# Performance work log

Hardware: AMD Instinct MI355X
Metric: run time of the kernel (lower is better)

## Reference

```python
import jax, jax.numpy as jnp
import numpy as np

N, D, R, NB, E = 50000, 128, 16, 10, 1600000
DECAY_RATE = 0.1
LN_EPS = 1e-5

def setup_inputs() -> dict:
    key = jax.random.key(0)
    ks = jax.random.split(key, 12)
    x = jax.random.normal(ks[0], (N, D), dtype=jnp.float32)
    edge_index = jax.random.randint(ks[1], (2, E), 0, N, dtype=jnp.int64)
    edge_type = jax.random.randint(ks[2], (E,), 0, R, dtype=jnp.int64)
    edge_time = jax.random.uniform(ks[3], (E,), dtype=jnp.float32)
    s = 1.0 / np.sqrt(D)
    basis = jax.random.normal(ks[4], (NB, D, D), dtype=jnp.float32) * s   # RGCN basis matrices
    comp = jax.random.normal(ks[5], (R, NB), dtype=jnp.float32) * (1.0 / np.sqrt(NB))
    root = jax.random.normal(ks[6], (D, D), dtype=jnp.float32) * s        # RGCN self-loop weight
    bias = jnp.zeros((D,), dtype=jnp.float32)
    tp_w = jax.random.normal(ks[7], (D, D), dtype=jnp.float32) * s        # time_proj
    tp_b = jnp.zeros((D,), dtype=jnp.float32)
    gamma = jnp.ones((D,), dtype=jnp.float32)
    beta = jnp.zeros((D,), dtype=jnp.float32)
    return {"x": x, "edge_index": edge_index, "edge_type": edge_type, "edge_time": edge_time,
            "basis": basis, "comp": comp, "root": root, "bias": bias,
            "tp_w": tp_w, "tp_b": tp_b, "gamma": gamma, "beta": beta}

def reference(x, edge_index, edge_type, edge_time, basis, comp, root, bias, tp_w, tp_b, gamma, beta):
    n, d = x.shape
    r = comp.shape[0]
    src, dst = edge_index[0], edge_index[1]
    # ---- RGCNConv (basis decomposition, per-relation mean aggregation) ----
    W = jnp.einsum('rb,bio->rio', comp, basis)                 # [R, D, D]
    msg = x[src]                                               # [E, D] gather
    seg = dst * r + edge_type                                  # combined (node, relation) segment id
    agg = jax.ops.segment_sum(msg, seg, num_segments=n * r)    # [N*R, D]
    cnt = jax.ops.segment_sum(jnp.ones_like(seg, dtype=x.dtype), seg, num_segments=n * r)
    agg = (agg / jnp.maximum(cnt, 1.0)[:, None]).reshape(n, r, d)  # per-relation mean
    x_rgcn = jnp.einsum('nrd,rdo->no', agg, W) + x @ root + bias
    # ---- exponential time decay weights, normalized to sum 1 ----
    td = edge_time.max() - edge_time
    td = td / (td.max() + 1e-8)
    w = jnp.exp(-DECAY_RATE * td)
    w = w / (w.sum() + 1e-8)
    # ---- time-decay aggregation (sum over relations == single scatter-add) ----
    agg_t = jax.ops.segment_sum(msg * w[:, None], dst, num_segments=n)
    deg = jax.ops.segment_sum(jnp.ones_like(dst, dtype=x.dtype), dst, num_segments=n)
    x_time = agg_t / jnp.clip(deg, 1.0)[:, None]
    # ---- combine, relu, (dropout=identity in eval), layernorm ----
    xc = x_rgcn + x_time @ tp_w + tp_b
    h = jax.nn.relu(xc)
    mu = h.mean(-1, keepdims=True)
    var = ((h - mu) ** 2).mean(-1, keepdims=True)
    return (h - mu) * jax.lax.rsqrt(var + LN_EPS) * gamma + beta
```

## Files before the change

kernel.cpp:

```cpp
#include <hip/hip_runtime.h>
#include <hip/hip_bf16.h>
#include <math.h>

#define NN 50000
#define DD 128
#define RR 16
#define NBASIS 10
#define NE 1600000
#define NSEG (NN * RR)
#define NSLICE 12
#define KTOT (NSLICE * DD)
#define DECAY 0.1f

#define NB_COARSE 782
#define NBLK_S 1024
#define EPB 1563
#define NHC (NB_COARSE * NBLK_S)
#define NPART2 (NHC / 1024)
#define FINE 1024
#define CAP 2560

typedef short bf16x8 __attribute__((ext_vector_type(8)));
typedef float f32x4 __attribute__((ext_vector_type(4)));
typedef float f32x2 __attribute__((ext_vector_type(2)));

__device__ __forceinline__ ushort f2b(float f) {
    unsigned u = __float_as_uint(f);
    unsigned r = (u + 0x7FFFu + ((u >> 16) & 1u)) >> 16;
    return (ushort)r;
}
__device__ __forceinline__ unsigned cvt_pk_bf16(float lo, float hi) {
    unsigned r;
    asm("v_cvt_pk_bf16_f32 %0, %1, %2" : "=v"(r) : "v"(lo), "v"(hi));
    return r;
}


#define XB_ITEMS (NN * (DD / 4))
#define PREP_ITEMS (XB_ITEMS + DD * KTOT)
__global__ __launch_bounds__(256) void k_s1(
    const int* __restrict__ edst, const float* __restrict__ t,
    const float* __restrict__ x, const float* __restrict__ basis,
    const float* __restrict__ root, const float* __restrict__ tp_w,
    unsigned* __restrict__ red, unsigned* __restrict__ Hc,
    ushort* __restrict__ xb, ushort* __restrict__ Bt3)
{
    const int bid = blockIdx.x;
    const int tid = threadIdx.x;
    if (bid < NBLK_S) {
        __shared__ unsigned h[NB_COARSE];
        for (int i = tid; i < NB_COARSE; i += 256) h[i] = 0u;
        __syncthreads();
        const int e0 = bid * EPB;
        const int e1 = (e0 + EPB < NE) ? e0 + EPB : NE;
        for (int e = e0 + tid; e < e1; e += 256) {
            int d = __builtin_nontemporal_load(edst + e);
            atomicAdd(&h[d >> 6], 1u);
        }
        __syncthreads();
        for (int i = tid; i < NB_COARSE; i += 256)
            Hc[i * NBLK_S + bid] = h[i];
        return;
    }
    if (bid < NBLK_S + 256) {
        __shared__ float smx[4], smn[4];
        float mx = 0.0f, mn = 1e30f;
        const int stride = 256 * 256;
        for (int i = (bid - NBLK_S) * 256 + tid; i < NE / 4; i += stride) {
            f32x4 v = __builtin_nontemporal_load(((const f32x4*)t) + i);
            mx = fmaxf(mx, fmaxf(fmaxf(v.x, v.y), fmaxf(v.z, v.w)));
            mn = fminf(mn, fminf(fminf(v.x, v.y), fminf(v.z, v.w)));
        }
        for (int o = 32; o >= 1; o >>= 1) {
            mx = fmaxf(mx, __shfl_down(mx, o, 64));
            mn = fminf(mn, __shfl_down(mn, o, 64));
        }
        if ((tid & 63) == 0) { smx[tid >> 6] = mx; smn[tid >> 6] = mn; }
        __syncthreads();
        if (tid == 0) {
            mx = fmaxf(fmaxf(smx[0], smx[1]), fmaxf(smx[2], smx[3]));
            mn = fminf(fminf(smn[0], smn[1]), fminf(smn[2], smn[3]));
            atomicMax(&red[0], __float_as_uint(mx));
            atomicMax(&red[1], ~__float_as_uint(mn));
        }
        return;
    }
    int idx = (bid - NBLK_S - 256) * 256 + tid;
    if (idx < XB_ITEMS) {
        f32x4 v = ((const f32x4*)x)[idx];
        uint2 o;
        o.x = cvt_pk_bf16(v.x, v.y);
        o.y = cvt_pk_bf16(v.z, v.w);
        ((uint2*)xb)[idx] = o;
        return;
    }
    int bidx = idx - XB_ITEMS;
    if (bidx >= DD * KTOT) return;
    int j = bidx / KTOT, k = bidx - j * KTOT;
    int s = k >> 7, d = k & 127;
    float v;
    if (s < NBASIS) {
        v = basis[(s * DD + d) * DD + j];
    } else if (s == NBASIS) {
        v = tp_w[d * DD + j];
    } else {
        v = root[d * DD + j];
    }
    Bt3[bidx] = f2b(v);
}

__global__ __launch_bounds__(1024) void k_scan1(unsigned* __restrict__ Hc,
                                                unsigned* __restrict__ part) {
    __shared__ unsigned sh[1024];
    int tid = threadIdx.x;
    int i = blockIdx.x * 1024 + tid;
    unsigned v = Hc[i];
    sh[tid] = v;
    __syncthreads();
    for (int off = 1; off < 1024; off <<= 1) {
        unsigned t = (tid >= off) ? sh[tid - off] : 0u;
        __syncthreads();
        sh[tid] += t;
        __syncthreads();
    }
    Hc[i] = sh[tid] - v;
    if (tid == 1023) part[blockIdx.x] = sh[1023];
}

__global__ __launch_bounds__(1024) void k_scan2(unsigned* __restrict__ part) {
    __shared__ unsigned sh[1024];
    int tid = threadIdx.x;
    unsigned v = (tid < NPART2) ? part[tid] : 0u;
    sh[tid] = v;
    __syncthreads();
    for (int off = 1; off < 1024; off <<= 1) {
        unsigned t = (tid >= off) ? sh[tid - off] : 0u;
        __syncthreads();
        sh[tid] += t;
        __syncthreads();
    }
    if (tid < NPART2) part[tid] = sh[tid] - v;
}

__global__ __launch_bounds__(1024) void k_scan3(unsigned* __restrict__ Hc,
                                                const unsigned* __restrict__ part) {
    int i = blockIdx.x * 1024 + threadIdx.x;
    Hc[i] += part[i >> 10];
}

__global__ __launch_bounds__(256) void k_s3(
    const int* __restrict__ esrc, const int* __restrict__ edst,
    const int* __restrict__ etype, const float* __restrict__ etime,
    const unsigned* __restrict__ Hc, unsigned* __restrict__ red,
    unsigned long long* __restrict__ tmp)
{
    __shared__ unsigned cur[NB_COARSE];
    __shared__ float ssum[4];
    const int bid = blockIdx.x;
    const int tid = threadIdx.x;
    for (int i = tid; i < NB_COARSE; i += 256)
        cur[i] = Hc[i * NBLK_S + bid];
    const float tmax = __uint_as_float(red[0]);
    const float tmin = __uint_as_float(~red[1]);
    const float rtd = -DECAY / (tmax - tmin + 1e-8f);
    __syncthreads();
    float s = 0.0f;
    const int e0 = bid * EPB;
    const int e1 = (e0 + EPB < NE) ? e0 + EPB : NE;
    for (int e = e0 + tid; e < e1; e += 256) {
        int d    = __builtin_nontemporal_load(edst + e);
        int ty   = __builtin_nontemporal_load(etype + e);
        int sv   = __builtin_nontemporal_load(esrc + e);
        float tv = __builtin_nontemporal_load(etime + e);
        float w = __expf((tmax - tv) * rtd);
        s += w;
        unsigned seg = (unsigned)(d * RR + ty);
        unsigned pos = atomicAdd(&cur[seg >> 10], 1u);
        unsigned lo = (unsigned)(sv & 0xFFFF) | ((unsigned)f2b(w) << 16);
        __builtin_nontemporal_store(
            ((unsigned long long)seg << 32) | lo, tmp + pos);
    }
    for (int o = 32; o >= 1; o >>= 1) s += __shfl_down(s, o, 64);
    if ((tid & 63) == 0) ssum[tid >> 6] = s;
    __syncthreads();
    if (tid == 0)
        atomicAdd(((float*)red) + 2, ssum[0] + ssum[1] + ssum[2] + ssum[3]);
}

__global__ __launch_bounds__(512) void k_s4(
    const unsigned long long* __restrict__ tmp, const unsigned* __restrict__ Hc,
    unsigned* __restrict__ srcw, unsigned* __restrict__ segptr)
{
    __shared__ unsigned long long recs[CAP];
    __shared__ unsigned hist[FINE];
    __shared__ unsigned excl[FINE];
    __shared__ unsigned curf[FINE];
    __shared__ unsigned sh[512];
    const int b = blockIdx.x;
    const int tid = threadIdx.x;
    const unsigned start = Hc[b * NBLK_S];
    const unsigned end   = (b + 1 < NB_COARSE) ? Hc[(b + 1) * NBLK_S] : (unsigned)NE;
    int n = (int)(end - start);
    if (n > CAP) n = CAP;
    for (int i = tid; i < FINE; i += 512) hist[i] = 0u;
    for (int i = tid; i < n; i += 512) recs[i] = tmp[start + i];
    __syncthreads();
    const unsigned base = (unsigned)b << 10;
    for (int i = tid; i < n; i += 512)
        atomicAdd(&hist[(unsigned)(recs[i] >> 32) - base], 1u);
    __syncthreads();
    unsigned a0 = hist[2 * tid], a1 = hist[2 * tid + 1];
    sh[tid] = a0 + a1;
    __syncthreads();
    for (int off = 1; off < 512; off <<= 1) {
        unsigned t = (tid >= off) ? sh[tid - off] : 0u;
        __syncthreads();
        sh[tid] += t;
        __syncthreads();
    }
    unsigned pe = sh[tid] - (a0 + a1);
    excl[2 * tid] = pe;          curf[2 * tid] = pe;
    excl[2 * tid + 1] = pe + a0; curf[2 * tid + 1] = pe + a0;
    __syncthreads();
    for (int i = tid; i < n; i += 512) {
        unsigned long long r = recs[i];
        unsigned p = atomicAdd(&curf[(unsigned)(r >> 32) - base], 1u);
        srcw[start + p] = (unsigned)r;
    }
    for (int i = tid; i < FINE; i += 512)
        segptr[(size_t)b * FINE + i] = start + excl[i];
}

__global__ __launch_bounds__(256) void k_gather(
    const ushort* __restrict__ xb, const unsigned* __restrict__ srcw,
    const unsigned* __restrict__ segptr, const unsigned* __restrict__ red,
    const float* __restrict__ comp,
    ushort* __restrict__ A2)
{
    const int wave = threadIdx.x >> 6, lane = threadIdx.x & 63;
    int dst0 = blockIdx.x * 4 + wave;
    if (dst0 >= NN) return;
    const int dst = __builtin_amdgcn_readfirstlane(dst0);
    const float sumw = ((const float*)red)[2];
    const unsigned s0 = (unsigned)dst * RR;
    const unsigned start = segptr[s0];
    const unsigned endAll = segptr[s0 + RR];
    const unsigned deg = endAll - start;
    unsigned* arow = (unsigned*)(A2 + (size_t)dst * KTOT);
    const unsigned* xbu = (const unsigned*)xb;

    f32x2 cb[NBASIS];
#pragma unroll
    for (int b = 0; b < NBASIS; ++b) cb[b] = (f32x2){0.f, 0.f};
    f32x2 acc = {0.f, 0.f}, xt = {0.f, 0.f};

    int r = 0;
    unsigned scur = start;
    unsigned endr = segptr[s0 + 1];
    unsigned e = start;

#define FLUSH_REL {                                                          \
        float scl = (endr > scur) ? (1.0f / (float)(endr - scur)) : 0.0f;    \
        f32x2 t = acc * scl;                                                 \
        _Pragma("unroll")                                                    \
        for (int b = 0; b < NBASIS; ++b)                                     \
            cb[b] += t * comp[r * NBASIS + b];                               \
        acc = (f32x2){0.f, 0.f}; scur = endr; ++r;                           \
        endr = (r < RR) ? segptr[s0 + r + 1] : 0xFFFFFFFFu; }

#define ACCUM(recq, pvq) {                                                   \
        float wgt = __uint_as_float((recq) & 0xFFFF0000u);                   \
        f32x2 v;                                                             \
        v.x = __uint_as_float((pvq) << 16);                                  \
        v.y = __uint_as_float((pvq) & 0xFFFF0000u);                          \
        acc += v;                                                            \
        xt += v * wgt; }

    while (e < endAll) {
        unsigned idx = e + (unsigned)lane;
        unsigned recv = srcw[(idx < endAll) ? idx : (endAll - 1u)];
        unsigned chunk = endAll - e;
        if (chunk > 64u) chunk = 64u;
        unsigned j = 0;
        for (; j + 8u <= chunk; j += 8u) {
            unsigned rec0 = (unsigned)__builtin_amdgcn_readlane((int)recv, (int)(j + 0));
            unsigned rec1 = (unsigned)__builtin_amdgcn_readlane((int)recv, (int)(j + 1));
            unsigned rec2 = (unsigned)__builtin_amdgcn_readlane((int)recv, (int)(j + 2));
            unsigned rec3 = (unsigned)__builtin_amdgcn_readlane((int)recv, (int)(j + 3));
            unsigned rec4 = (unsigned)__builtin_amdgcn_readlane((int)recv, (int)(j + 4));
            unsigned rec5 = (unsigned)__builtin_amdgcn_readlane((int)recv, (int)(j + 5));
            unsigned rec6 = (unsigned)__builtin_amdgcn_readlane((int)recv, (int)(j + 6));
            unsigned rec7 = (unsigned)__builtin_amdgcn_readlane((int)recv, (int)(j + 7));
            unsigned pv0 = xbu[((rec0 & 0xFFFFu) << 6) + lane];
            unsigned pv1 = xbu[((rec1 & 0xFFFFu) << 6) + lane];
            unsigned pv2 = xbu[((rec2 & 0xFFFFu) << 6) + lane];
            unsigned pv3 = xbu[((rec3 & 0xFFFFu) << 6) + lane];
            unsigned pv4 = xbu[((rec4 & 0xFFFFu) << 6) + lane];
            unsigned pv5 = xbu[((rec5 & 0xFFFFu) << 6) + lane];
            unsigned pv6 = xbu[((rec6 & 0xFFFFu) << 6) + lane];
            unsigned pv7 = xbu[((rec7 & 0xFFFFu) << 6) + lane];
            while (e >= endr) FLUSH_REL; ACCUM(rec0, pv0); ++e;
            while (e >= endr) FLUSH_REL; ACCUM(rec1, pv1); ++e;
            while (e >= endr) FLUSH_REL; ACCUM(rec2, pv2); ++e;
            while (e >= endr) FLUSH_REL; ACCUM(rec3, pv3); ++e;
            while (e >= endr) FLUSH_REL; ACCUM(rec4, pv4); ++e;
            while (e >= endr) FLUSH_REL; ACCUM(rec5, pv5); ++e;
            while (e >= endr) FLUSH_REL; ACCUM(rec6, pv6); ++e;
            while (e >= endr) FLUSH_REL; ACCUM(rec7, pv7); ++e;
        }
        for (; j < chunk; ++j) {
            unsigned rc = (unsigned)__builtin_amdgcn_readlane((int)recv, (int)j);
            unsigned pv = xbu[((rc & 0xFFFFu) << 6) + lane];
            while (e >= endr) FLUSH_REL;
            ACCUM(rc, pv);
            ++e;
        }
    }
    while (r < RR) FLUSH_REL;

#pragma unroll
    for (int b = 0; b < NBASIS; ++b)
        __builtin_nontemporal_store(cvt_pk_bf16(cb[b].x, cb[b].y),
                                    arow + b * 64 + lane);

    float s2 = 1.0f / ((sumw + 1e-8f) * fmaxf((float)deg, 1.0f));
    __builtin_nontemporal_store(cvt_pk_bf16(xt.x * s2, xt.y * s2),
                                arow + NBASIS * 64 + lane);
    __builtin_nontemporal_store(
        ((const unsigned*)(xb + (size_t)dst * DD))[lane],
        arow + (NBASIS + 1) * 64 + lane);
#undef FLUSH_REL
#undef ACCUM
}

__global__ __launch_bounds__(256) void k_fgemm(
    const ushort* __restrict__ A2, const ushort* __restrict__ Bt3,
    const float* __restrict__ bias, const float* __restrict__ tpb,
    const float* __restrict__ gamma, const float* __restrict__ beta,
    float* __restrict__ out)
{
    __shared__ unsigned Bs[2][4096];

    const int tid = threadIdx.x;
    const int w = tid >> 6, lane = tid & 63;
    const int quad = lane >> 4, l16 = lane & 15;
    const int n0 = blockIdx.x * 64;

    f32x4 acc[8];
#pragma unroll
    for (int ct = 0; ct < 8; ++ct) acc[ct] = (f32x4){0.f, 0.f, 0.f, 0.f};

    const ushort* arow = A2 + (size_t)(n0 + w * 16 + l16) * KTOT + quad * 8;
    const int srow = lane >> 3;
    const int sc   = lane & 7;

#define STAGE(buf, itv) {                                                    \
        const int k0_ = (itv) * 64;                                          \
        _Pragma("unroll")                                                    \
        for (int i_ = 0; i_ < 4; ++i_) {                                     \
            const int cid_ = i_ * 4 + w;                                     \
            const int row_ = cid_ * 8 + srow;                                \
            const int ck_  = sc ^ (row_ & 7);                                \
            const ushort* gb_ = Bt3 + (size_t)row_ * KTOT + k0_ + ck_ * 8;   \
            __builtin_amdgcn_global_load_lds(                                \
                (const __attribute__((address_space(1))) unsigned*)gb_,      \
                (__attribute__((address_space(3))) unsigned*)&Bs[buf][cid_ * 256], \
                16, 0, 0);                                                   \
        } }

    STAGE(0, 0);
    bf16x8 afp0 = *(const bf16x8*)(arow);
    bf16x8 afp1 = *(const bf16x8*)(arow + 32);
    __syncthreads();

    const int NIT = KTOT / 64;
    for (int it = 0; it < NIT; ++it) {
        if (it + 1 < NIT) STAGE((it + 1) & 1, it + 1);
        bf16x8 af0 = afp0, af1 = afp1;
        if (it + 1 < NIT) {
            afp0 = *(const bf16x8*)(arow + (it + 1) * 64);
            afp1 = *(const bf16x8*)(arow + (it + 1) * 64 + 32);
        }
        const unsigned* Bp = &Bs[it & 1][0];
#pragma unroll
        for (int ct = 0; ct < 8; ++ct) {
            const int rB = ct * 16 + l16;
            bf16x8 b0 = *(const bf16x8*)&Bp[rB * 32 + ((quad ^ (rB & 7)) << 2)];
            bf16x8 b1 = *(const bf16x8*)&Bp[rB * 32 + (((4 + quad) ^ (rB & 7)) << 2)];
            acc[ct] = __builtin_amdgcn_mfma_f32_16x16x32_bf16(af0, b0, acc[ct], 0, 0, 0);
            acc[ct] = __builtin_amdgcn_mfma_f32_16x16x32_bf16(af1, b1, acc[ct], 0, 0, 0);
        }
        __syncthreads();
    }
#undef STAGE

    float bc[8], gc[8], be[8];
#pragma unroll
    for (int ct = 0; ct < 8; ++ct) {
        int col = ct * 16 + l16;
        bc[ct] = bias[col] + tpb[col];
        gc[ct] = gamma[col];
        be[ct] = beta[col];
    }
    float s[4] = {0, 0, 0, 0}, q[4] = {0, 0, 0, 0};
#pragma unroll
    for (int ct = 0; ct < 8; ++ct)
#pragma unroll
        for (int i = 0; i < 4; ++i) {
            float v = fmaxf(acc[ct][i] + bc[ct], 0.0f);
            acc[ct][i] = v;
            s[i] += v;
            q[i] = fmaf(v, v, q[i]);
        }
#pragma unroll
    for (int off = 1; off < 16; off <<= 1)
#pragma unroll
        for (int i = 0; i < 4; ++i) {
            s[i] += __shfl_xor(s[i], off, 64);
            q[i] += __shfl_xor(q[i], off, 64);
        }
#pragma unroll
    for (int i = 0; i < 4; ++i) {
        const int row = n0 + w * 16 + quad * 4 + i;
        float mu  = s[i] * (1.0f / DD);
        float var = q[i] * (1.0f / DD) - mu * mu;
        float inv = rsqrtf(var + 1e-5f);
        if (row < NN) {
#pragma unroll
            for (int ct = 0; ct < 8; ++ct)
                __builtin_nontemporal_store(
                    (acc[ct][i] - mu) * inv * gc[ct] + be[ct],
                    out + (size_t)row * DD + ct * 16 + l16);
        }
    }
}

extern "C" void kernel_launch(void* const* d_in, const int* in_sizes, int n_in,
                              void* d_out, int out_size, void* d_ws, size_t ws_size,
                              hipStream_t stream)
{
    const float* x     = (const float*)d_in[0];
    const int*   ei    = (const int*)d_in[1];
    const int*   etype = (const int*)d_in[2];
    const float* etime = (const float*)d_in[3];
    const float* basis = (const float*)d_in[4];
    const float* comp  = (const float*)d_in[5];
    const float* root  = (const float*)d_in[6];
    const float* bias  = (const float*)d_in[7];
    const float* tp_w  = (const float*)d_in[8];
    const float* tp_b  = (const float*)d_in[9];
    const float* gamma = (const float*)d_in[10];
    const float* beta  = (const float*)d_in[11];
    float* out = (float*)d_out;

    char* ws = (char*)d_ws;
    size_t off = 0;
    auto alloc = [&](size_t bytes) -> void* {
        void* p = ws + off;
        off = (off + bytes + 255) & ~(size_t)255;
        return p;
    };
    unsigned* red    = (unsigned*)alloc(256);
    unsigned* Hc     = (unsigned*)alloc((size_t)NHC * 4);
    unsigned* part   = (unsigned*)alloc(1024 * 4);
    unsigned* srcw   = (unsigned*)alloc((size_t)NE * 4);
    unsigned long long* tmp = (unsigned long long*)alloc((size_t)NE * 8);
    unsigned* segptr = (unsigned*)alloc((size_t)(NB_COARSE * FINE) * 4);
    ushort*   xb     = (ushort*)alloc((size_t)NN * DD * 2);
    ushort*   Bt3    = (ushort*)alloc((size_t)DD * KTOT * 2);
    ushort*   A2     = (ushort*)alloc((size_t)50048 * KTOT * 2);
    (void)ws_size;

    const int* esrc = ei;
    const int* edst = ei + NE;

    (void)hipMemsetAsync(red, 0, 256, stream);

    const int prep_blocks = (PREP_ITEMS + 255) / 256;
    hipLaunchKernelGGL(k_s1, dim3(NBLK_S + 256 + prep_blocks), dim3(256), 0, stream,
                       edst, etime, x, basis, root, tp_w, red, Hc, xb, Bt3);

    hipLaunchKernelGGL(k_scan1, dim3(NPART2), dim3(1024), 0, stream, Hc, part);
    hipLaunchKernelGGL(k_scan2, dim3(1), dim3(1024), 0, stream, part);
    hipLaunchKernelGGL(k_scan3, dim3(NPART2), dim3(1024), 0, stream, Hc, part);

    hipLaunchKernelGGL(k_s3, dim3(NBLK_S), dim3(256), 0, stream,
                       esrc, edst, etype, etime, Hc, red, tmp);

    hipLaunchKernelGGL(k_s4, dim3(NB_COARSE), dim3(512), 0, stream,
                       tmp, Hc, srcw, segptr);

    hipLaunchKernelGGL(k_gather, dim3((NN + 3) / 4), dim3(256), 0, stream,
                       xb, srcw, segptr, red, comp, A2);

    hipLaunchKernelGGL(k_fgemm, dim3((50048 + 63) / 64), dim3(256), 0, stream,
                       A2, Bt3, bias, tp_b, gamma, beta, out);
}
```

Before: 344.7 us.

## Fuse gather and GEMM+LayerNorm into one kernel using LDS-staged A rows

Merges the gather kernel and the fused GEMM/LayerNorm kernel into one 1024-thread block kernel. Each block gathers 16 destination rows into padded LDS, then 16 waves split the 128 output columns and two K halves and run MFMA with B read straight from global memory. Partial sums and LayerNorm statistics are reduced through LDS. This removes the write and re-read of the large A2 intermediate, but B is no longer staged in LDS and is reloaded by every block, and occupancy may fall because of the large blocks and LDS use.

```diff
diff --git a/kernel.cpp b/kernel.cpp
--- a/kernel.cpp
+++ b/kernel.cpp
@@ -7,7 +7,6 @@
 #define RR 16
 #define NBASIS 10
 #define NE 1600000
-#define NSEG (NN * RR)
 #define NSLICE 12
 #define KTOT (NSLICE * DD)
 #define DECAY 0.1f
@@ -19,6 +18,8 @@
 #define NPART2 (NHC / 1024)
 #define FINE 1024
 #define CAP 2560
+
+#define APAD 772
 
 typedef short bf16x8 __attribute__((ext_vector_type(8)));
 typedef float f32x4 __attribute__((ext_vector_type(4)));
@@ -231,41 +232,49 @@
         segptr[(size_t)b * FINE + i] = start + excl[i];
 }
 
-__global__ __launch_bounds__(256) void k_gather(
+__global__ __launch_bounds__(1024, 4) void k_gg(
     const ushort* __restrict__ xb, const unsigned* __restrict__ srcw,
     const unsigned* __restrict__ segptr, const unsigned* __restrict__ red,
-    const float* __restrict__ comp,
-    ushort* __restrict__ A2)
+    const float* __restrict__ comp, const ushort* __restrict__ Bt3,
+    const float* __restrict__ bias, const float* __restrict__ tpb,
+    const float* __restrict__ gamma, const float* __restrict__ beta,
+    float* __restrict__ out)
 {
-    const int wave = threadIdx.x >> 6, lane = threadIdx.x & 63;
-    int dst0 = blockIdx.x * 4 + wave;
-    if (dst0 >= NN) return;
-    const int dst = __builtin_amdgcn_readfirstlane(dst0);
-    const float sumw = ((const float*)red)[2];
-    const unsigned s0 = (unsigned)dst * RR;
-    const unsigned start = segptr[s0];
-    const unsigned endAll = segptr[s0 + RR];
-    const unsigned deg = endAll - start;
-    unsigned* arow = (unsigned*)(A2 + (size_t)dst * KTOT);
-    const unsigned* xbu = (const unsigned*)xb;
-
-    f32x2 cb[NBASIS];
-#pragma unroll
-    for (int b = 0; b < NBASIS; ++b) cb[b] = (f32x2){0.f, 0.f};
-    f32x2 acc = {0.f, 0.f}, xt = {0.f, 0.f};
-
-    int r = 0;
-    unsigned scur = start;
-    unsigned endr = segptr[s0 + 1];
-    unsigned e = start;
+    __shared__ unsigned As[16 * APAD];
+    __shared__ f32x4 racc[8][64];
+    __shared__ float rs[128], rq[128];
+
+    const int tid = threadIdx.x;
+    const int w = tid >> 6, lane = tid & 63;
+    const int l16 = lane & 15, quad = lane >> 4;
+
+    {
+        const int dst = __builtin_amdgcn_readfirstlane(blockIdx.x * 16 + w);
+        const float sumw = ((const float*)red)[2];
+        const unsigned s0 = (unsigned)dst * RR;
+        const unsigned start = segptr[s0];
+        const unsigned endAll = segptr[s0 + RR];
+        const unsigned deg = endAll - start;
+        unsigned* arow = &As[w * APAD];
+        const unsigned* xbu = (const unsigned*)xb;
+
+        f32x2 cb[NBASIS];
+#pragma unroll
+        for (int b = 0; b < NBASIS; ++b) cb[b] = (f32x2){0.f, 0.f};
+        f32x2 acc2 = {0.f, 0.f}, xt = {0.f, 0.f};
+
+        int r = 0;
+        unsigned scur = start;
+        unsigned endr = segptr[s0 + 1];
+        unsigned e = start;
 
 #define FLUSH_REL {                                                          \
         float scl = (endr > scur) ? (1.0f / (float)(endr - scur)) : 0.0f;    \
-        f32x2 t = acc * scl;                                                 \
+        f32x2 t = acc2 * scl;                                                \
         _Pragma("unroll")                                                    \
         for (int b = 0; b < NBASIS; ++b)                                     \
             cb[b] += t * comp[r * NBASIS + b];                               \
-        acc = (f32x2){0.f, 0.f}; scur = endr; ++r;                           \
+        acc2 = (f32x2){0.f, 0.f}; scur = endr; ++r;                          \
         endr = (r < RR) ? segptr[s0 + r + 1] : 0xFFFFFFFFu; }
 
 #define ACCUM(recq, pvq) {                                                   \
@@ -273,145 +282,89 @@
         f32x2 v;                                                             \
         v.x = __uint_as_float((pvq) << 16);                                  \
         v.y = __uint_as_float((pvq) & 0xFFFF0000u);                          \
-        acc += v;                                                            \
+        acc2 += v;                                                           \
         xt += v * wgt; }
 
-    while (e < endAll) {
-        unsigned idx = e + (unsigned)lane;
-        unsigned recv = srcw[(idx < endAll) ? idx : (endAll - 1u)];
-        unsigned chunk = endAll - e;
-        if (chunk > 64u) chunk = 64u;
-        unsigned j = 0;
-        for (; j + 8u <= chunk; j += 8u) {
-            unsigned rec0 = (unsigned)__builtin_amdgcn_readlane((int)recv, (int)(j + 0));
-            unsigned rec1 = (unsigned)__builtin_amdgcn_readlane((int)recv, (int)(j + 1));
-            unsigned rec2 = (unsigned)__builtin_amdgcn_readlane((int)recv, (int)(j + 2));
-            unsigned rec3 = (unsigned)__builtin_amdgcn_readlane((int)recv, (int)(j + 3));
-            unsigned rec4 = (unsigned)__builtin_amdgcn_readlane((int)recv, (int)(j + 4));
-            unsigned rec5 = (unsigned)__builtin_amdgcn_readlane((int)recv, (int)(j + 5));
-            unsigned rec6 = (unsigned)__builtin_amdgcn_readlane((int)recv, (int)(j + 6));
-            unsigned rec7 = (unsigned)__builtin_amdgcn_readlane((int)recv, (int)(j + 7));
-            unsigned pv0 = xbu[((rec0 & 0xFFFFu) << 6) + lane];
-            unsigned pv1 = xbu[((rec1 & 0xFFFFu) << 6) + lane];
-            unsigned pv2 = xbu[((rec2 & 0xFFFFu) << 6) + lane];
-            unsigned pv3 = xbu[((rec3 & 0xFFFFu) << 6) + lane];
-            unsigned pv4 = xbu[((rec4 & 0xFFFFu) << 6) + lane];
-            unsigned pv5 = xbu[((rec5 & 0xFFFFu) << 6) + lane];
-            unsigned pv6 = xbu[((rec6 & 0xFFFFu) << 6) + lane];
-            unsigned pv7 = xbu[((rec7 & 0xFFFFu) << 6) + lane];
-            while (e >= endr) FLUSH_REL; ACCUM(rec0, pv0); ++e;
-            while (e >= endr) FLUSH_REL; ACCUM(rec1, pv1); ++e;
-            while (e >= endr) FLUSH_REL; ACCUM(rec2, pv2); ++e;
-            while (e >= endr) FLUSH_REL; ACCUM(rec3, pv3); ++e;
-            while (e >= endr) FLUSH_REL; ACCUM(rec4, pv4); ++e;
-            while (e >= endr) FLUSH_REL; ACCUM(rec5, pv5); ++e;
-            while (e >= endr) FLUSH_REL; ACCUM(rec6, pv6); ++e;
-            while (e >= endr) FLUSH_REL; ACCUM(rec7, pv7); ++e;
-        }
-        for (; j < chunk; ++j) {
-            unsigned rc = (unsigned)__builtin_amdgcn_readlane((int)recv, (int)j);
-            unsigned pv = xbu[((rc & 0xFFFFu) << 6) + lane];
-            while (e >= endr) FLUSH_REL;
-            ACCUM(rc, pv);
-            ++e;
-        }
-    }
-    while (r < RR) FLUSH_REL;
-
-#pragma unroll
-    for (int b = 0; b < NBASIS; ++b)
-        __builtin_nontemporal_store(cvt_pk_bf16(cb[b].x, cb[b].y),
-                                    arow + b * 64 + lane);
-
-    float s2 = 1.0f / ((sumw + 1e-8f) * fmaxf((float)deg, 1.0f));
-    __builtin_nontemporal_store(cvt_pk_bf16(xt.x * s2, xt.y * s2),
-                                arow + NBASIS * 64 + lane);
-    __builtin_nontemporal_store(
-        ((const unsigned*)(xb + (size_t)dst * DD))[lane],
-        arow + (NBASIS + 1) * 64 + lane);
+        while (e < endAll) {
+            unsigned idx = e + (unsigned)lane;
+            unsigned recv = srcw[(idx < endAll) ? idx : (endAll - 1u)];
+            unsigned chunk = endAll - e;
+            if (chunk > 64u) chunk = 64u;
+            unsigned j = 0;
+            for (; j + 8u <= chunk; j += 8u) {
+                unsigned rec0 = (unsigned)__builtin_amdgcn_readlane((int)recv, (int)(j + 0));
+                unsigned rec1 = (unsigned)__builtin_amdgcn_readlane((int)recv, (int)(j + 1));
+                unsigned rec2 = (unsigned)__builtin_amdgcn_readlane((int)recv, (int)(j + 2));
+                unsigned rec3 = (unsigned)__builtin_amdgcn_readlane((int)recv, (int)(j + 3));
+                unsigned rec4 = (unsigned)__builtin_amdgcn_readlane((int)recv, (int)(j + 4));
+                unsigned rec5 = (unsigned)__builtin_amdgcn_readlane((int)recv, (int)(j + 5));
+                unsigned rec6 = (unsigned)__builtin_amdgcn_readlane((int)recv, (int)(j + 6));
+                unsigned rec7 = (unsigned)__builtin_amdgcn_readlane((int)recv, (int)(j + 7));
+                unsigned pv0 = xbu[((rec0 & 0xFFFFu) << 6) + lane];
+                unsigned pv1 = xbu[((rec1 & 0xFFFFu) << 6) + lane];
+                unsigned pv2 = xbu[((rec2 & 0xFFFFu) << 6) + lane];
+                unsigned pv3 = xbu[((rec3 & 0xFFFFu) << 6) + lane];
+                unsigned pv4 = xbu[((rec4 & 0xFFFFu) << 6) + lane];
+                unsigned pv5 = xbu[((rec5 & 0xFFFFu) << 6) + lane];
+                unsigned pv6 = xbu[((rec6 & 0xFFFFu) << 6) + lane];
+                unsigned pv7 = xbu[((rec7 & 0xFFFFu) << 6) + lane];
+                while (e >= endr) FLUSH_REL; ACCUM(rec0, pv0); ++e;
+                while (e >= endr) FLUSH_REL; ACCUM(rec1, pv1); ++e;
+                while (e >= endr) FLUSH_REL; ACCUM(rec2, pv2); ++e;
+                while (e >= endr) FLUSH_REL; ACCUM(rec3, pv3); ++e;
+                while (e >= endr) FLUSH_REL; ACCUM(rec4, pv4); ++e;
+                while (e >= endr) FLUSH_REL; ACCUM(rec5, pv5); ++e;
+                while (e >= endr) FLUSH_REL; ACCUM(rec6, pv6); ++e;
+                while (e >= endr) FLUSH_REL; ACCUM(rec7, pv7); ++e;
+            }
+            for (; j < chunk; ++j) {
+                unsigned rc = (unsigned)__builtin_amdgcn_readlane((int)recv, (int)j);
+                unsigned pv = xbu[((rc & 0xFFFFu) << 6) + lane];
+                while (e >= endr) FLUSH_REL;
+                ACCUM(rc, pv);
+                ++e;
+            }
+        }
+        while (r < RR) FLUSH_REL;
+
+#pragma unroll
+        for (int b = 0; b < NBASIS; ++b)
+            arow[b * 64 + lane] = cvt_pk_bf16(cb[b].x, cb[b].y);
+        float s2 = 1.0f / ((sumw + 1e-8f) * fmaxf((float)deg, 1.0f));
+        arow[NBASIS * 64 + lane] = cvt_pk_bf16(xt.x * s2, xt.y * s2);
+        arow[(NBASIS + 1) * 64 + lane] =
+            ((const unsigned*)(xb + (size_t)dst * DD))[lane];
 #undef FLUSH_REL
 #undef ACCUM
-}
-
-__global__ __launch_bounds__(256) void k_fgemm(
-    const ushort* __restrict__ A2, const ushort* __restrict__ Bt3,
-    const float* __restrict__ bias, const float* __restrict__ tpb,
-    const float* __restrict__ gamma, const float* __restrict__ beta,
-    float* __restrict__ out)
-{
-    __shared__ unsigned Bs[2][4096];
-
-    const int tid = threadIdx.x;
-    const int w = tid >> 6, lane = tid & 63;
-    const int quad = lane >> 4, l16 = lane & 15;
-    const int n0 = blockIdx.x * 64;
-
-    f32x4 acc[8];
-#pragma unroll
-    for (int ct = 0; ct < 8; ++ct) acc[ct] = (f32x4){0.f, 0.f, 0.f, 0.f};
-
-    const ushort* arow = A2 + (size_t)(n0 + w * 16 + l16) * KTOT + quad * 8;
-    const int srow = lane >> 3;
-    const int sc   = lane & 7;
-
-#define STAGE(buf, itv) {                                                    \
-        const int k0_ = (itv) * 64;                                          \
-        _Pragma("unroll")                                                    \
-        for (int i_ = 0; i_ < 4; ++i_) {                                     \
-            const int cid_ = i_ * 4 + w;                                     \
-            const int row_ = cid_ * 8 + srow;                                \
-            const int ck_  = sc ^ (row_ & 7);                                \
-            const ushort* gb_ = Bt3 + (size_t)row_ * KTOT + k0_ + ck_ * 8;   \
-            __builtin_amdgcn_global_load_lds(                                \
-                (const __attribute__((address_space(1))) unsigned*)gb_,      \
-                (__attribute__((address_space(3))) unsigned*)&Bs[buf][cid_ * 256], \
-                16, 0, 0);                                                   \
-        } }
-
-    STAGE(0, 0);
-    bf16x8 afp0 = *(const bf16x8*)(arow);
-    bf16x8 afp1 = *(const bf16x8*)(arow + 32);
-    __syncthreads();
-
-    const int NIT = KTOT / 64;
-    for (int it = 0; it < NIT; ++it) {
-        if (it + 1 < NIT) STAGE((it + 1) & 1, it + 1);
-        bf16x8 af0 = afp0, af1 = afp1;
-        if (it + 1 < NIT) {
-            afp0 = *(const bf16x8*)(arow + (it + 1) * 64);
-            afp1 = *(const bf16x8*)(arow + (it + 1) * 64 + 32);
-        }
-        const unsigned* Bp = &Bs[it & 1][0];
-#pragma unroll
-        for (int ct = 0; ct < 8; ++ct) {
-            const int rB = ct * 16 + l16;
-            bf16x8 b0 = *(const bf16x8*)&Bp[rB * 32 + ((quad ^ (rB & 7)) << 2)];
-            bf16x8 b1 = *(const bf16x8*)&Bp[rB * 32 + (((4 + quad) ^ (rB & 7)) << 2)];
-            acc[ct] = __builtin_amdgcn_mfma_f32_16x16x32_bf16(af0, b0, acc[ct], 0, 0, 0);
-            acc[ct] = __builtin_amdgcn_mfma_f32_16x16x32_bf16(af1, b1, acc[ct], 0, 0, 0);
-        }
-        __syncthreads();
-    }
-#undef STAGE
-
-    float bc[8], gc[8], be[8];
-#pragma unroll
-    for (int ct = 0; ct < 8; ++ct) {
-        int col = ct * 16 + l16;
-        bc[ct] = bias[col] + tpb[col];
-        gc[ct] = gamma[col];
-        be[ct] = beta[col];
-    }
-    float s[4] = {0, 0, 0, 0}, q[4] = {0, 0, 0, 0};
-#pragma unroll
-    for (int ct = 0; ct < 8; ++ct)
-#pragma unroll
-        for (int i = 0; i < 4; ++i) {
-            float v = fmaxf(acc[ct][i] + bc[ct], 0.0f);
-            acc[ct][i] = v;
-            s[i] += v;
-            q[i] = fmaf(v, v, q[i]);
-        }
+    }
+    __syncthreads();
+
+    const int ct = w & 7, kh = w >> 3;
+    const int col = ct * 16 + l16;
+    f32x4 acc = (f32x4){0.f, 0.f, 0.f, 0.f};
+    {
+        const ushort* bcol = Bt3 + (size_t)col * KTOT + kh * 768 + quad * 8;
+        const int abase = l16 * APAD + kh * 384 + quad * 4;
+#pragma unroll
+        for (int kc = 0; kc < 24; ++kc) {
+            bf16x8 af = *(const bf16x8*)&As[abase + kc * 16];
+            bf16x8 bf = *(const bf16x8*)(bcol + kc * 32);
+            acc = __builtin_amdgcn_mfma_f32_16x16x32_bf16(af, bf, acc, 0, 0, 0);
+        }
+    }
+
+    if (w >= 8) racc[ct][lane] = acc;
+    __syncthreads();
+    if (w < 8) acc += racc[ct][lane];
+
+    float bc = bias[col] + tpb[col];
+    float gc = gamma[col], be = beta[col];
+    float s[4], q[4];
+#pragma unroll
+    for (int i = 0; i < 4; ++i) {
+        float v = fmaxf(acc[i] + bc, 0.0f);
+        acc[i] = v; s[i] = v; q[i] = v * v;
+    }
 #pragma unroll
     for (int off = 1; off < 16; off <<= 1)
 #pragma unroll
@@ -419,18 +372,27 @@
             s[i] += __shfl_xor(s[i], off, 64);
             q[i] += __shfl_xor(q[i], off, 64);
         }
-#pragma unroll
-    for (int i = 0; i < 4; ++i) {
-        const int row = n0 + w * 16 + quad * 4 + i;
-        float mu  = s[i] * (1.0f / DD);
-        float var = q[i] * (1.0f / DD) - mu * mu;
-        float inv = rsqrtf(var + 1e-5f);
-        if (row < NN) {
-#pragma unroll
-            for (int ct = 0; ct < 8; ++ct)
-                __builtin_nontemporal_store(
-                    (acc[ct][i] - mu) * inv * gc[ct] + be[ct],
-                    out + (size_t)row * DD + ct * 16 + l16);
+    if (w < 8 && l16 == 0) {
+#pragma unroll
+        for (int i = 0; i < 4; ++i) {
+            rs[ct * 16 + quad * 4 + i] = s[i];
+            rq[ct * 16 + quad * 4 + i] = q[i];
+        }
+    }
+    __syncthreads();
+    if (w < 8) {
+#pragma unroll
+        for (int i = 0; i < 4; ++i) {
+            const int rowl = quad * 4 + i;
+            float S = 0.f, Q = 0.f;
+#pragma unroll
+            for (int c = 0; c < 8; ++c) { S += rs[c * 16 + rowl]; Q += rq[c * 16 + rowl]; }
+            float mu  = S * (1.0f / DD);
+            float var = Q * (1.0f / DD) - mu * mu;
+            float inv = rsqrtf(var + 1e-5f);
+            __builtin_nontemporal_store(
+                (acc[i] - mu) * inv * gc + be,
+                out + (size_t)(blockIdx.x * 16 + rowl) * DD + col);
         }
     }
 }
@@ -468,7 +430,6 @@
     unsigned* segptr = (unsigned*)alloc((size_t)(NB_COARSE * FINE) * 4);
     ushort*   xb     = (ushort*)alloc((size_t)NN * DD * 2);
     ushort*   Bt3    = (ushort*)alloc((size_t)DD * KTOT * 2);
-    ushort*   A2     = (ushort*)alloc((size_t)50048 * KTOT * 2);
     (void)ws_size;
 
     const int* esrc = ei;
@@ -490,9 +451,7 @@
     hipLaunchKernelGGL(k_s4, dim3(NB_COARSE), dim3(512), 0, stream,
                        tmp, Hc, srcw, segptr);
 
-    hipLaunchKernelGGL(k_gather, dim3((NN + 3) / 4), dim3(256), 0, stream,
-                       xb, srcw, segptr, red, comp, A2);
-
-    hipLaunchKernelGGL(k_fgemm, dim3((50048 + 63) / 64), dim3(256), 0, stream,
-                       A2, Bt3, bias, tp_b, gamma, beta, out);
-}
+    hipLaunchKernelGGL(k_gg, dim3(NN / 16), dim3(1024), 0, stream,
+                       xb, srcw, segptr, red, comp, Bt3,
+                       bias, tp_b, gamma, beta, out);
+}
```

Result: slower. 480.7 us (+39.4%).
